# Kernel tuning notes

Measured on AMD Instinct MI355X. Metric: run time of the kernel, lower is better.

Reference implementation:

```python
import jax, jax.numpy as jnp
import numpy as np

N_NODES = 50000
N_EDGES = 800000
NFEAT = 256
NHID = 128
NCLASS = 64
LEAKY_SLOPE = 0.01  # torch F.leaky_relu default


def setup_inputs() -> dict:
    key = jax.random.key(0)
    ks = jax.random.split(key, 7)
    x = jax.random.normal(ks[0], (N_NODES, NFEAT), dtype=jnp.float32)
    edge_src = jax.random.randint(ks[1], (N_EDGES,), 0, N_NODES)
    edge_dst = jax.random.randint(ks[2], (N_EDGES,), 0, N_NODES)
    edge_w = jax.random.uniform(ks[3], (N_EDGES,), dtype=jnp.float32)
    W1 = jax.random.normal(ks[4], (NFEAT, NHID), dtype=jnp.float32) * (1.0 / np.sqrt(NFEAT))
    W2 = jax.random.normal(ks[5], (NHID, NHID), dtype=jnp.float32) * (1.0 / np.sqrt(NHID))
    W3 = jax.random.uniform(ks[6], (NHID, NCLASS), dtype=jnp.float32,
                            minval=-1.0 / np.sqrt(NCLASS), maxval=1.0 / np.sqrt(NCLASS))
    return {"x": x, "edge_src": edge_src, "edge_dst": edge_dst, "edge_w": edge_w,
            "W1": W1, "W2": W2, "W3": W3}


def reference(x, edge_src, edge_dst, edge_w, W1, W2, W3):
    n = x.shape[0]

    def spmm(h):
        # sparse adj @ h via gather + weighted scatter-add over edges
        msgs = h[edge_src] * edge_w[:, None]           # [E, d]
        return jax.ops.segment_sum(msgs, edge_dst, num_segments=n)

    x1 = jax.nn.leaky_relu(spmm(x @ W1), negative_slope=LEAKY_SLOPE)  # gc1 + leaky_relu
    x3 = spmm(x1 @ W2)                                                # gc2
    Y = jax.nn.sigmoid(x3 @ W3)                                       # multilabel head
    return (Y, x3)
```

## Files before the change

kernel.cpp:

```cpp
#include <hip/hip_runtime.h>
#include <hip/hip_bf16.h>


constexpr int N_NODES = 50000;
constexpr int N_EDGES = 800000;
constexpr int NFEAT = 256;
constexpr int NHID = 128;
constexpr int NCLASS = 64;
constexpr int EW = 64;

typedef __attribute__((ext_vector_type(8))) short short8;
typedef __attribute__((ext_vector_type(4))) float f32x4;

__device__ __forceinline__ unsigned short f32_to_bf16_rne(float f) {
  unsigned u = __float_as_uint(f);
  unsigned r = u + 0x7fffu + ((u >> 16) & 1u);
  return (unsigned short)(r >> 16);
}
__device__ __forceinline__ float bf16_to_f32(unsigned short s) {
  return __uint_as_float(((unsigned)s) << 16);
}

template <int K, int N>
__device__ __forceinline__ void pack_dev(const float* __restrict__ W,
                                         short* __restrict__ Bh,
                                         short* __restrict__ Bl, int blk) {
  int idx = blk * 256 + threadIdx.x;
  constexpr int NFRAG = (K / 32) * (N / 16);
  if (idx >= NFRAG * 64) return;
  int l = idx & 63;
  int f = idx >> 6;
  int kb = f / (N / 16), nt = f % (N / 16);
  int g = l >> 4;
  int n = nt * 16 + (l & 15);
#pragma unroll
  for (int j = 0; j < 8; ++j) {
    int k = kb * 32 + g * 8 + j;
    float v = W[(size_t)k * N + n];
    unsigned short h = f32_to_bf16_rne(v);
    Bh[((size_t)f * 64 + l) * 8 + j] = (short)h;
    Bl[((size_t)f * 64 + l) * 8 + j] = (short)f32_to_bf16_rne(v - bf16_to_f32(h));
  }
}

__global__ __launch_bounds__(256) void prep(const float* __restrict__ W1,
                                            const float* __restrict__ W2,
                                            const float* __restrict__ W3,
                                            short* W1h, short* W1l, short* W2h,
                                            short* W2l, short* W3h, short* W3l,
                                            int* __restrict__ cnt) {
  int b = blockIdx.x;
  if (b < 196) {
    int i = b * 256 + threadIdx.x;
    if (i < N_NODES) cnt[i] = 0;
  } else if (b < 212) {
    pack_dev<NFEAT, NHID>(W1, W1h, W1l, b - 196);
  } else if (b < 220) {
    pack_dev<NHID, NHID>(W2, W2h, W2l, b - 212);
  } else {
    pack_dev<NHID, NCLASS>(W3, W3h, W3l, b - 220);
  }
}

template <int K, int N, bool A_BF16, bool SIGMOID, bool OUT_BF16>
__device__ __forceinline__ void gemm_body(int bx, const void* __restrict__ Av,
                                          const short* __restrict__ Bh,
                                          const short* __restrict__ Bl,
                                          void* __restrict__ Cv, int M) {
  constexpr int WCOL = N / 2;
  constexpr int F = WCOL / 16;
  const int tid = threadIdx.x;
  const int wid = tid >> 6;
  const int lane = tid & 63;
  const int g = lane >> 4;
  const int brow = bx * 32 + (wid >> 1) * 16;
  const int col0 = (wid & 1) * WCOL;
  const int row_a = brow + (lane & 15);

  f32x4 acc[F];
#pragma unroll
  for (int i = 0; i < F; ++i) acc[i] = (f32x4){0.f, 0.f, 0.f, 0.f};

#pragma unroll
  for (int kb = 0; kb < K / 32; ++kb) {
    const int ca = kb * 32 + g * 8;
    short8 ah, al;
    if (A_BF16) {
      const unsigned short* A = (const unsigned short*)Av;
      if (row_a < M) {
        ah = *reinterpret_cast<const short8*>(A + (size_t)row_a * K + ca);
      } else {
        ah = (short8){0, 0, 0, 0, 0, 0, 0, 0};
      }
    } else {
      const float* A = (const float*)Av;
      float4 a0 = {0.f, 0.f, 0.f, 0.f}, a1 = {0.f, 0.f, 0.f, 0.f};
      if (row_a < M) {
        a0 = *reinterpret_cast<const float4*>(A + (size_t)row_a * K + ca);
        a1 = *reinterpret_cast<const float4*>(A + (size_t)row_a * K + ca + 4);
      }
      float av[8] = {a0.x, a0.y, a0.z, a0.w, a1.x, a1.y, a1.z, a1.w};
#pragma unroll
      for (int j = 0; j < 8; ++j) {
        float v = av[j];
        unsigned short h = f32_to_bf16_rne(v);
        ah[j] = (short)h;
        al[j] = (short)f32_to_bf16_rne(v - bf16_to_f32(h));
      }
    }
#pragma unroll
    for (int nt = 0; nt < F; ++nt) {
      int f = kb * (N / 16) + (col0 >> 4) + nt;
      short8 bh = *reinterpret_cast<const short8*>(Bh + ((size_t)f * 64 + lane) * 8);
      short8 bl = *reinterpret_cast<const short8*>(Bl + ((size_t)f * 64 + lane) * 8);
      acc[nt] = __builtin_amdgcn_mfma_f32_16x16x32_bf16(ah, bh, acc[nt], 0, 0, 0);
      if (!A_BF16)
        acc[nt] = __builtin_amdgcn_mfma_f32_16x16x32_bf16(al, bh, acc[nt], 0, 0, 0);
      acc[nt] = __builtin_amdgcn_mfma_f32_16x16x32_bf16(ah, bl, acc[nt], 0, 0, 0);
    }
  }

#pragma unroll
  for (int nt = 0; nt < F; ++nt) {
    int c = col0 + nt * 16 + (lane & 15);
#pragma unroll
    for (int reg = 0; reg < 4; ++reg) {
      int r = brow + g * 4 + reg;
      if (r < M) {
        float v = acc[nt][reg];
        if (SIGMOID) v = 1.f / (1.f + __expf(-v));
        if (OUT_BF16) {
          ((unsigned short*)Cv)[(size_t)r * N + c] = f32_to_bf16_rne(v);
        } else {
          ((float*)Cv)[(size_t)r * N + c] = v;
        }
      }
    }
  }
}

template <int K, int N, bool A_BF16, bool SIGMOID, bool OUT_BF16>
__global__ __launch_bounds__(256) void gemm_mfma(const void* __restrict__ Av,
                                                 const short* __restrict__ Bh,
                                                 const short* __restrict__ Bl,
                                                 void* __restrict__ Cv, int M) {
  gemm_body<K, N, A_BF16, SIGMOID, OUT_BF16>(blockIdx.x, Av, Bh, Bl, Cv, M);
}

constexpr int GB1 = (N_NODES + 31) / 32;

__global__ __launch_bounds__(256) void fused_gemm1_fill(
    const float* __restrict__ x, const short* __restrict__ W1h,
    const short* __restrict__ W1l, unsigned short* __restrict__ hb,
    const int* __restrict__ src, const int* __restrict__ dst,
    const float* __restrict__ w, int* __restrict__ cnt,
    float2* __restrict__ ell) {
  int b = blockIdx.x;
  if (b < GB1) {
    gemm_body<NFEAT, NHID, false, false, true>(b, x, W1h, W1l, hb, N_NODES);
  } else {
    int e = (b - GB1) * 256 + threadIdx.x;
    if (e >= N_EDGES) return;
    int d = dst[e];
    int slot = atomicAdd(&cnt[d], 1);
    if (slot < EW) {
      float2 p;
      p.x = __int_as_float(src[e]);
      p.y = w[e];
      ell[(size_t)d * EW + slot] = p;
    }
  }
}

template <bool LEAKY, bool OUT_BF16>
__global__ __launch_bounds__(256) void spmm_ell(const unsigned* __restrict__ hb,
                                                const float2* __restrict__ ell,
                                                const int* __restrict__ cnt,
                                                void* __restrict__ outv, int nNodes) {
  int node = blockIdx.x * 4 + (threadIdx.x >> 6);
  if (node >= nNodes) return;
  int lane = threadIdx.x & 63;
  int n = cnt[node];
  if (n > EW) n = EW;
  float2 mydesc = ell[(size_t)node * EW + lane];
  int msrc = __float_as_int(mydesc.x);
  float mw = mydesc.y;

  float ax = 0.f, ay = 0.f;
  int j = 0;
  for (; j + 8 <= n; j += 8) {
    unsigned u[8];
    float ww[8];
#pragma unroll
    for (int t = 0; t < 8; ++t) {
      int s = __shfl(msrc, j + t, 64);
      ww[t] = __shfl(mw, j + t, 64);
      u[t] = hb[(size_t)s * 64 + lane];
    }
#pragma unroll
    for (int t = 0; t < 8; ++t) {
      ax += ww[t] * __uint_as_float(u[t] << 16);
      ay += ww[t] * __uint_as_float(u[t] & 0xffff0000u);
    }
  }
  for (; j < n; ++j) {
    int s = __shfl(msrc, j, 64);
    float wwj = __shfl(mw, j, 64);
    unsigned uj = hb[(size_t)s * 64 + lane];
    ax += wwj * __uint_as_float(uj << 16);
    ay += wwj * __uint_as_float(uj & 0xffff0000u);
  }

  if (LEAKY) {
    ax = (ax > 0.f) ? ax : 0.01f * ax;
    ay = (ay > 0.f) ? ay : 0.01f * ay;
  }
  if (OUT_BF16) {
    unsigned pk = ((unsigned)f32_to_bf16_rne(ay) << 16) | (unsigned)f32_to_bf16_rne(ax);
    ((unsigned*)outv)[(size_t)node * 64 + lane] = pk;
  } else {
    float2 o;
    o.x = ax;
    o.y = ay;
    ((float2*)outv)[(size_t)node * 64 + lane] = o;
  }
}

extern "C" void kernel_launch(void* const* d_in, const int* in_sizes, int n_in,
                              void* d_out, int out_size, void* d_ws, size_t ws_size,
                              hipStream_t stream) {
  const float* x = (const float*)d_in[0];
  const int* edge_src = (const int*)d_in[1];
  const int* edge_dst = (const int*)d_in[2];
  const float* edge_w = (const float*)d_in[3];
  const float* W1 = (const float*)d_in[4];
  const float* W2 = (const float*)d_in[5];
  const float* W3 = (const float*)d_in[6];

  float* Y = (float*)d_out;
  float* x3 = (float*)d_out + (size_t)N_NODES * NCLASS;

  unsigned* hb = (unsigned*)d_ws;
  unsigned* x1b = hb + (size_t)N_NODES * 64;
  float2* ell = (float2*)(x1b + (size_t)N_NODES * 64);
  int* cnt = (int*)(ell + (size_t)N_NODES * EW);
  short* W1h = (short*)(cnt + N_NODES);
  short* W1l = W1h + NFEAT * NHID;
  short* W2h = W1l + NFEAT * NHID;
  short* W2l = W2h + NHID * NHID;
  short* W3h = W2l + NHID * NHID;
  short* W3l = W3h + NHID * NCLASS;

  const int edge_blocks = (N_EDGES + 255) / 256;
  const int node_grid = (N_NODES + 3) / 4;
  const int gemm_grid = (N_NODES + 31) / 32;

  prep<<<224, 256, 0, stream>>>(W1, W2, W3, W1h, W1l, W2h, W2l, W3h, W3l, cnt);

  fused_gemm1_fill<<<GB1 + edge_blocks, 256, 0, stream>>>(
      x, W1h, W1l, (unsigned short*)hb, edge_src, edge_dst, edge_w, cnt, ell);

  spmm_ell<true, true><<<node_grid, 256, 0, stream>>>(hb, ell, cnt, x1b, N_NODES);

  gemm_mfma<NHID, NHID, true, false, true>
      <<<gemm_grid, 256, 0, stream>>>(x1b, W2h, W2l, hb, N_NODES);

  spmm_ell<false, false><<<node_grid, 256, 0, stream>>>(hb, ell, cnt, x3, N_NODES);

  gemm_mfma<NHID, NCLASS, false, true, false>
      <<<gemm_grid, 256, 0, stream>>>(x3, W3h, W3l, Y, N_NODES);
}
```

Measured before the change: 258.6 us.

## Fuse GCN pipeline into cooperative megakernel and pack ELL entries to 32 bits

Replaces the six separate kernel launches with one persistent cooperative kernel. Each phase runs as a grid-stride loop and the phases are separated by grid.sync, which removes per-launch gaps and tail effects between stages. ELL entries shrink from a float2 to a single 32-bit word holding a 16-bit source index and an fp16 weight, halving the adjacency bytes written by the fill and read by both SpMMs. GEMM1 and edge-fill work items are also interleaved so both run together, and a multi-kernel fallback is kept in case the cooperative launch fails. The costs are grid-wide barrier overhead, lower occupancy from the fixed persistent grid, and reduced edge-weight precision, with source indices now limited to 16 bits.

```diff
diff --git a/kernel.cpp b/kernel.cpp
--- a/kernel.cpp
+++ b/kernel.cpp
@@ -1,5 +1,9 @@
 #include <hip/hip_runtime.h>
 #include <hip/hip_bf16.h>
+#include <hip/hip_fp16.h>
+#include <hip/hip_cooperative_groups.h>
+
+namespace cg = cooperative_groups;
 
 
 constexpr int N_NODES = 50000;
@@ -8,6 +12,10 @@
 constexpr int NHID = 128;
 constexpr int NCLASS = 64;
 constexpr int EW = 64;
+
+constexpr int GB1 = (N_NODES + 31) / 32;
+constexpr int EDGE_BLOCKS = (N_EDGES + 255) / 256;
+constexpr int NODE_BLOCKS = (N_NODES + 3) / 4;
 
 typedef __attribute__((ext_vector_type(8))) short short8;
 typedef __attribute__((ext_vector_type(4))) float f32x4;
@@ -43,13 +51,12 @@
   }
 }
 
-__global__ __launch_bounds__(256) void prep(const float* __restrict__ W1,
-                                            const float* __restrict__ W2,
-                                            const float* __restrict__ W3,
-                                            short* W1h, short* W1l, short* W2h,
-                                            short* W2l, short* W3h, short* W3l,
-                                            int* __restrict__ cnt) {
-  int b = blockIdx.x;
+__device__ __forceinline__ void prep_body(int b, const float* __restrict__ W1,
+                                          const float* __restrict__ W2,
+                                          const float* __restrict__ W3, short* W1h,
+                                          short* W1l, short* W2h, short* W2l,
+                                          short* W3h, short* W3l,
+                                          int* __restrict__ cnt) {
   if (b < 196) {
     int i = b * 256 + threadIdx.x;
     if (i < N_NODES) cnt[i] = 0;
@@ -139,76 +146,73 @@
   }
 }
 
-template <int K, int N, bool A_BF16, bool SIGMOID, bool OUT_BF16>
-__global__ __launch_bounds__(256) void gemm_mfma(const void* __restrict__ Av,
-                                                 const short* __restrict__ Bh,
-                                                 const short* __restrict__ Bl,
-                                                 void* __restrict__ Cv, int M) {
-  gemm_body<K, N, A_BF16, SIGMOID, OUT_BF16>(blockIdx.x, Av, Bh, Bl, Cv, M);
-}
-
-constexpr int GB1 = (N_NODES + 31) / 32;
-
-__global__ __launch_bounds__(256) void fused_gemm1_fill(
-    const float* __restrict__ x, const short* __restrict__ W1h,
-    const short* __restrict__ W1l, unsigned short* __restrict__ hb,
-    const int* __restrict__ src, const int* __restrict__ dst,
-    const float* __restrict__ w, int* __restrict__ cnt,
-    float2* __restrict__ ell) {
-  int b = blockIdx.x;
-  if (b < GB1) {
-    gemm_body<NFEAT, NHID, false, false, true>(b, x, W1h, W1l, hb, N_NODES);
-  } else {
-    int e = (b - GB1) * 256 + threadIdx.x;
-    if (e >= N_EDGES) return;
+__device__ __forceinline__ void fill_body(int chunk, const int* __restrict__ src,
+                                          const int* __restrict__ dst,
+                                          const float* __restrict__ w,
+                                          int* __restrict__ cnt,
+                                          unsigned* __restrict__ ell) {
+  int e = chunk * 256 + threadIdx.x;
+  if (e < N_EDGES) {
     int d = dst[e];
     int slot = atomicAdd(&cnt[d], 1);
     if (slot < EW) {
-      float2 p;
-      p.x = __int_as_float(src[e]);
-      p.y = w[e];
-      ell[(size_t)d * EW + slot] = p;
-    }
+      unsigned short hw = __half_as_ushort(__float2half_rn(w[e]));
+      ell[(size_t)d * EW + slot] = ((unsigned)hw << 16) | (unsigned)src[e];
+    }
+  }
+}
+
+__device__ __forceinline__ void p1_body(int wk, const float* __restrict__ x,
+                                        const short* __restrict__ W1h,
+                                        const short* __restrict__ W1l,
+                                        unsigned short* __restrict__ hb,
+                                        const int* __restrict__ src,
+                                        const int* __restrict__ dst,
+                                        const float* __restrict__ w,
+                                        int* __restrict__ cnt,
+                                        unsigned* __restrict__ ell) {
+  int g = wk / 3, r = wk % 3;
+  if (r == 0) {
+    gemm_body<NFEAT, NHID, false, false, true>(g, x, W1h, W1l, hb, N_NODES);
+  } else {
+    fill_body(2 * g + r - 1, src, dst, w, cnt, ell);
   }
 }
 
 template <bool LEAKY, bool OUT_BF16>
-__global__ __launch_bounds__(256) void spmm_ell(const unsigned* __restrict__ hb,
-                                                const float2* __restrict__ ell,
-                                                const int* __restrict__ cnt,
-                                                void* __restrict__ outv, int nNodes) {
-  int node = blockIdx.x * 4 + (threadIdx.x >> 6);
-  if (node >= nNodes) return;
+__device__ __forceinline__ void spmm_body(int bx, const unsigned* __restrict__ hb,
+                                          const unsigned* __restrict__ ell,
+                                          const int* __restrict__ cnt,
+                                          void* __restrict__ outv) {
+  int node = bx * 4 + (threadIdx.x >> 6);
+  if (node >= N_NODES) return;
   int lane = threadIdx.x & 63;
   int n = cnt[node];
   if (n > EW) n = EW;
-  float2 mydesc = ell[(size_t)node * EW + lane];
-  int msrc = __float_as_int(mydesc.x);
-  float mw = mydesc.y;
+  unsigned mydesc = ell[(size_t)node * EW + lane];
 
   float ax = 0.f, ay = 0.f;
   int j = 0;
   for (; j + 8 <= n; j += 8) {
-    unsigned u[8];
-    float ww[8];
+    unsigned dsc[8], u[8];
 #pragma unroll
     for (int t = 0; t < 8; ++t) {
-      int s = __shfl(msrc, j + t, 64);
-      ww[t] = __shfl(mw, j + t, 64);
-      u[t] = hb[(size_t)s * 64 + lane];
+      dsc[t] = __shfl(mydesc, j + t, 64);
+      u[t] = hb[(size_t)(dsc[t] & 0xffffu) * 64 + lane];
     }
 #pragma unroll
     for (int t = 0; t < 8; ++t) {
-      ax += ww[t] * __uint_as_float(u[t] << 16);
-      ay += ww[t] * __uint_as_float(u[t] & 0xffff0000u);
+      float wv = __half2float(__ushort_as_half((unsigned short)(dsc[t] >> 16)));
+      ax += wv * __uint_as_float(u[t] << 16);
+      ay += wv * __uint_as_float(u[t] & 0xffff0000u);
     }
   }
   for (; j < n; ++j) {
-    int s = __shfl(msrc, j, 64);
-    float wwj = __shfl(mw, j, 64);
-    unsigned uj = hb[(size_t)s * 64 + lane];
-    ax += wwj * __uint_as_float(uj << 16);
-    ay += wwj * __uint_as_float(uj & 0xffff0000u);
+    unsigned dj = __shfl(mydesc, j, 64);
+    unsigned uj = hb[(size_t)(dj & 0xffffu) * 64 + lane];
+    float wv = __half2float(__ushort_as_half((unsigned short)(dj >> 16)));
+    ax += wv * __uint_as_float(uj << 16);
+    ay += wv * __uint_as_float(uj & 0xffff0000u);
   }
 
   if (LEAKY) {
@@ -224,6 +228,87 @@
     o.y = ay;
     ((float2*)outv)[(size_t)node * 64 + lane] = o;
   }
+}
+
+__global__ __launch_bounds__(256, 4) void gcn_mega(
+    const float* __restrict__ x, const int* __restrict__ edge_src,
+    const int* __restrict__ edge_dst, const float* __restrict__ edge_w,
+    const float* __restrict__ W1, const float* __restrict__ W2,
+    const float* __restrict__ W3, float* __restrict__ Y, unsigned* __restrict__ ws) {
+  cg::grid_group grid = cg::this_grid();
+  const int G = gridDim.x;
+
+  unsigned* hb = ws;
+  unsigned* x1b = hb + (size_t)N_NODES * 64;
+  unsigned* ell = x1b + (size_t)N_NODES * 64;
+  int* cnt = (int*)(ell + (size_t)N_NODES * EW);
+  short* W1h = (short*)(cnt + N_NODES);
+  short* W1l = W1h + NFEAT * NHID;
+  short* W2h = W1l + NFEAT * NHID;
+  short* W2l = W2h + NHID * NHID;
+  short* W3h = W2l + NHID * NHID;
+  short* W3l = W3h + NHID * NCLASS;
+  float* x3 = Y + (size_t)N_NODES * NCLASS;
+
+  for (int b = blockIdx.x; b < 224; b += G)
+    prep_body(b, W1, W2, W3, W1h, W1l, W2h, W2l, W3h, W3l, cnt);
+  grid.sync();
+
+  for (int wk = blockIdx.x; wk < GB1 + EDGE_BLOCKS; wk += G)
+    p1_body(wk, x, W1h, W1l, (unsigned short*)hb, edge_src, edge_dst, edge_w, cnt, ell);
+  grid.sync();
+
+  for (int b = blockIdx.x; b < NODE_BLOCKS; b += G)
+    spmm_body<true, true>(b, hb, ell, cnt, x1b);
+  grid.sync();
+
+  for (int b = blockIdx.x; b < GB1; b += G)
+    gemm_body<NHID, NHID, true, false, true>(b, x1b, W2h, W2l, hb, N_NODES);
+  grid.sync();
+
+  for (int b = blockIdx.x; b < NODE_BLOCKS; b += G)
+    spmm_body<false, false>(b, hb, ell, cnt, x3);
+  grid.sync();
+
+  for (int b = blockIdx.x; b < GB1; b += G)
+    gemm_body<NHID, NCLASS, false, true, false>(b, x3, W3h, W3l, Y, N_NODES);
+}
+
+__global__ __launch_bounds__(256) void prep_k(const float* __restrict__ W1,
+                                              const float* __restrict__ W2,
+                                              const float* __restrict__ W3, short* W1h,
+                                              short* W1l, short* W2h, short* W2l,
+                                              short* W3h, short* W3l,
+                                              int* __restrict__ cnt) {
+  prep_body(blockIdx.x, W1, W2, W3, W1h, W1l, W2h, W2l, W3h, W3l, cnt);
+}
+
+__global__ __launch_bounds__(256) void p1_k(const float* __restrict__ x,
+                                            const short* __restrict__ W1h,
+                                            const short* __restrict__ W1l,
+                                            unsigned short* __restrict__ hb,
+                                            const int* __restrict__ src,
+                                            const int* __restrict__ dst,
+                                            const float* __restrict__ w,
+                                            int* __restrict__ cnt,
+                                            unsigned* __restrict__ ell) {
+  p1_body(blockIdx.x, x, W1h, W1l, hb, src, dst, w, cnt, ell);
+}
+
+template <bool LEAKY, bool OUT_BF16>
+__global__ __launch_bounds__(256) void spmm_k(const unsigned* __restrict__ hb,
+                                              const unsigned* __restrict__ ell,
+                                              const int* __restrict__ cnt,
+                                              void* __restrict__ outv) {
+  spmm_body<LEAKY, OUT_BF16>(blockIdx.x, hb, ell, cnt, outv);
+}
+
+template <int K, int N, bool A_BF16, bool SIGMOID, bool OUT_BF16>
+__global__ __launch_bounds__(256) void gemm_k(const void* __restrict__ Av,
+                                              const short* __restrict__ Bh,
+                                              const short* __restrict__ Bl,
+                                              void* __restrict__ Cv, int M) {
+  gemm_body<K, N, A_BF16, SIGMOID, OUT_BF16>(blockIdx.x, Av, Bh, Bl, Cv, M);
 }
 
 extern "C" void kernel_launch(void* const* d_in, const int* in_sizes, int n_in,
@@ -236,13 +321,12 @@
   const float* W1 = (const float*)d_in[4];
   const float* W2 = (const float*)d_in[5];
   const float* W3 = (const float*)d_in[6];
-
   float* Y = (float*)d_out;
-  float* x3 = (float*)d_out + (size_t)N_NODES * NCLASS;
-
-  unsigned* hb = (unsigned*)d_ws;
+  unsigned* ws = (unsigned*)d_ws;
+
+  unsigned* hb = ws;
   unsigned* x1b = hb + (size_t)N_NODES * 64;
-  float2* ell = (float2*)(x1b + (size_t)N_NODES * 64);
+  unsigned* ell = x1b + (size_t)N_NODES * 64;
   int* cnt = (int*)(ell + (size_t)N_NODES * EW);
   short* W1h = (short*)(cnt + N_NODES);
   short* W1l = W1h + NFEAT * NHID;
@@ -250,23 +334,31 @@
   short* W2l = W2h + NHID * NHID;
   short* W3h = W2l + NHID * NHID;
   short* W3l = W3h + NHID * NCLASS;
-
-  const int edge_blocks = (N_EDGES + 255) / 256;
-  const int node_grid = (N_NODES + 3) / 4;
-  const int gemm_grid = (N_NODES + 31) / 32;
-
-  prep<<<224, 256, 0, stream>>>(W1, W2, W3, W1h, W1l, W2h, W2l, W3h, W3l, cnt);
-
-  fused_gemm1_fill<<<GB1 + edge_blocks, 256, 0, stream>>>(
-      x, W1h, W1l, (unsigned short*)hb, edge_src, edge_dst, edge_w, cnt, ell);
-
-  spmm_ell<true, true><<<node_grid, 256, 0, stream>>>(hb, ell, cnt, x1b, N_NODES);
-
-  gemm_mfma<NHID, NHID, true, false, true>
-      <<<gemm_grid, 256, 0, stream>>>(x1b, W2h, W2l, hb, N_NODES);
-
-  spmm_ell<false, false><<<node_grid, 256, 0, stream>>>(hb, ell, cnt, x3, N_NODES);
-
-  gemm_mfma<NHID, NCLASS, false, true, false>
-      <<<gemm_grid, 256, 0, stream>>>(x3, W3h, W3l, Y, N_NODES);
-}
+  float* x3 = Y + (size_t)N_NODES * NCLASS;
+
+  hipError_t rc = hipErrorUnknown;
+  int maxB = 0, nCU = 0;
+  if (hipOccupancyMaxActiveBlocksPerMultiprocessor(&maxB, (const void*)gcn_mega, 256,
+                                                   0) == hipSuccess &&
+      hipDeviceGetAttribute(&nCU, hipDeviceAttributeMultiprocessorCount, 0) ==
+          hipSuccess &&
+      maxB > 0 && nCU > 0) {
+    dim3 grid(maxB * nCU);
+    void* args[] = {(void*)&x,  (void*)&edge_src, (void*)&edge_dst,
+                    (void*)&edge_w, (void*)&W1,   (void*)&W2,
+                    (void*)&W3, (void*)&Y,        (void*)&ws};
+    rc = hipLaunchCooperativeKernel((const void*)gcn_mega, grid, dim3(256), args, 0,
+                                    stream);
+  }
+  if (rc == hipSuccess) return;
+
+  prep_k<<<224, 256, 0, stream>>>(W1, W2, W3, W1h, W1l, W2h, W2l, W3h, W3l, cnt);
+  p1_k<<<GB1 + EDGE_BLOCKS, 256, 0, stream>>>(x, W1h, W1l, (unsigned short*)hb,
+                                              edge_src, edge_dst, edge_w, cnt, ell);
+  spmm_k<true, true><<<NODE_BLOCKS, 256, 0, stream>>>(hb, ell, cnt, x1b);
+  gemm_k<NHID, NHID, true, false, true>
+      <<<GB1, 256, 0, stream>>>(x1b, W2h, W2l, hb, N_NODES);
+  spmm_k<false, false><<<NODE_BLOCKS, 256, 0, stream>>>(hb, ell, cnt, x3);
+  gemm_k<NHID, NCLASS, false, true, false>
+      <<<GB1, 256, 0, stream>>>(x3, W3h, W3l, Y, N_NODES);
+}
```

After: 693.6 us. +168.2%, slower.
